# Kernel optimization log

Hardware: AMD Instinct MI355X
Metric: run time of the kernel (lower is better)

Reference implementation:

```python
import jax, jax.numpy as jnp
import numpy as np

EOS_IDX = 2
B, S, T = 512, 64, 32
V, E, H, DENC, L = 128, 256, 512, 1024, 2


def setup_inputs() -> dict:
    key = jax.random.key(0)
    ks = jax.random.split(key, 24)
    s = 0.02
    inp = {
        "encoder_out": jax.random.normal(ks[0], (B, S, DENC), jnp.float32),
        "h0": jax.random.normal(ks[1], (L, B, H), jnp.float32),
        "c0": jax.random.normal(ks[2], (L, B, H), jnp.float32),
        "targets": jax.random.randint(ks[3], (B, T), 0, V),
        "mask": jax.random.randint(ks[4], (B, S), 0, 2).astype(jnp.int32),
        # parameters
        "emb": jax.random.normal(ks[5], (V, E), jnp.float32) * s,
        "W_enc": jax.random.normal(ks[6], (H, DENC), jnp.float32) * s,
        "W_dec": jax.random.normal(ks[7], (H, H), jnp.float32) * s,
        "v": jax.random.normal(ks[8], (H,), jnp.float32) * s,
        "W_ih0": jax.random.normal(ks[9], (4 * H, E + DENC), jnp.float32) * s,
        "W_hh0": jax.random.normal(ks[10], (4 * H, H), jnp.float32) * s,
        "b_ih0": jax.random.normal(ks[11], (4 * H,), jnp.float32) * s,
        "b_hh0": jax.random.normal(ks[12], (4 * H,), jnp.float32) * s,
        "W_ih1": jax.random.normal(ks[13], (4 * H, H), jnp.float32) * s,
        "W_hh1": jax.random.normal(ks[14], (4 * H, H), jnp.float32) * s,
        "b_ih1": jax.random.normal(ks[15], (4 * H,), jnp.float32) * s,
        "b_hh1": jax.random.normal(ks[16], (4 * H,), jnp.float32) * s,
        "W_out": jax.random.normal(ks[17], (V, H + DENC + E), jnp.float32) * s,
        "b_out": jax.random.normal(ks[18], (V,), jnp.float32) * s,
    }
    # guarantee at least one valid source position per row
    inp["mask"] = inp["mask"].at[:, 0].set(1)
    return inp


def _lstm_cell(x, h, c, W_ih, W_hh, b_ih, b_hh):
    gates = x @ W_ih.T + b_ih + h @ W_hh.T + b_hh  # (B, 4H)
    i, f, g, o = jnp.split(gates, 4, axis=-1)      # torch gate order i,f,g,o
    c_new = jax.nn.sigmoid(f) * c + jax.nn.sigmoid(i) * jnp.tanh(g)
    h_new = jax.nn.sigmoid(o) * jnp.tanh(c_new)
    return h_new, c_new


def reference(encoder_out, h0, c0, targets, mask,
              emb, W_enc, W_dec, v,
              W_ih0, W_hh0, b_ih0, b_hh0,
              W_ih1, W_hh1, b_ih1, b_hh1,
              W_out, b_out):
    # teacher_forcing_ratio = 1.0: input tokens are [EOS, targets[:, :-1]]
    tokens = jnp.concatenate(
        [jnp.full((targets.shape[0], 1), EOS_IDX, dtype=targets.dtype),
         targets[:, :-1]], axis=1)                       # (B, T)
    embedded = emb[tokens]                               # (B, T, E)
    enc_proj = jnp.einsum('bsd,hd->bsh', encoder_out, W_enc)  # precompute W_enc(encoder_out)
    mask_b = mask > 0                                    # (B, S)

    def step(carry, x_emb):                              # x_emb: (B, E)
        h, c = carry                                     # each (L, B, H)
        h_top = h[-1]                                    # (B, H)
        dec_proj = h_top @ W_dec.T                       # (B, H)
        energy = jnp.tanh(dec_proj[:, None, :] + enc_proj)   # (B, S, H)
        score = jnp.einsum('bsh,h->bs', energy, v)       # (B, S)
        score = jnp.where(mask_b, score, -jnp.inf)
        weights = jax.nn.softmax(score, axis=-1)         # (B, S)
        context = jnp.einsum('bs,bsd->bd', weights, encoder_out)  # (B, DENC)
        x = jnp.concatenate([x_emb, context], axis=-1)   # (B, E+DENC)
        h0n, c0n = _lstm_cell(x, h[0], c[0], W_ih0, W_hh0, b_ih0, b_hh0)
        h1n, c1n = _lstm_cell(h0n, h[1], c[1], W_ih1, W_hh1, b_ih1, b_hh1)
        pred = jnp.concatenate([h1n, context, x_emb], axis=-1) @ W_out.T + b_out  # (B, V)
        return (jnp.stack([h0n, h1n]), jnp.stack([c0n, c1n])), pred

    (_, _), preds = jax.lax.scan(step, (h0, c0), jnp.swapaxes(embedded, 0, 1))
    return jnp.swapaxes(preds, 0, 1)                     # (B, T, V)
```

## Files before the change

### kernel.cpp

```cpp
#include <hip/hip_runtime.h>
#include <math.h>

#define BB 512
#define SS 64
#define TT 32
#define VV 128
#define EE 256
#define HH 512
#define DENC 1024
#define BH (BB*HH)
#define XW0 1792
#define XW1 1024
#define PW  1792
#define G4H 2048

typedef __attribute__((ext_vector_type(8))) short bf16x8;
typedef __attribute__((ext_vector_type(4))) short bf16x4;
typedef __attribute__((ext_vector_type(4))) float f32x4;

__device__ __forceinline__ float sigf(float x){ return 1.f/(1.f+expf(-x)); }
__device__ __forceinline__ float bf2f(short s){
  return __uint_as_float(((unsigned)(unsigned short)s) << 16);
}
__device__ __forceinline__ short f2bf(float f){
  unsigned u = __float_as_uint(f);
  return (short)((u + 0x7FFF + ((u>>16)&1)) >> 16);
}
__device__ __forceinline__ float tanh_fast(float x){
  x = fminf(fmaxf(x, -15.f), 15.f);
  float e = __expf(2.f*x);
  return (e - 1.f) / (e + 1.f);
}

template<int BM, int BN>
struct GemmPipe {
  static constexpr int LA = 72;
  static __device__ __forceinline__ void run(short* Asb, short* Bsb,
      const short* __restrict__ A, const short* __restrict__ Bt, int K,
      int rowBase, int colBase, int tid, f32x4 acc[BM/32][BN/32])
  {
    constexpr int FI = BM/32, FJ = BN/32, ACH = BM/32, BCH = BN/32;
    const int lane = tid & 63, wave = tid >> 6;
    const int ml = lane & 15, kq = lane >> 4;
    const int wm = (wave >> 1)*(BM/2), wn = (wave & 1)*(BN/2);
    const int arow = (tid*ACH) >> 3, acol = ((tid*ACH) & 7)*8;
    const int brow = (tid*BCH) >> 3, bcol = ((tid*BCH) & 7)*8;
    const short* Ap = A + (size_t)(rowBase+arow)*K + acol;
    const short* Bp = Bt + (size_t)(colBase+brow)*K + bcol;
    bf16x8 ar[ACH], br[BCH];
    #pragma unroll
    for (int c = 0; c < ACH; ++c) ar[c] = *(const bf16x8*)(Ap + c*8);
    #pragma unroll
    for (int c = 0; c < BCH; ++c) br[c] = *(const bf16x8*)(Bp + c*8);
    const int nIter = K >> 6;
    for (int i = 0; i < nIter; ++i) {
      short* Ab = Asb + (i&1)*(BM*LA);
      short* Bb = Bsb + (i&1)*(BN*LA);
      #pragma unroll
      for (int c = 0; c < ACH; ++c) *(bf16x8*)&Ab[arow*LA + acol + c*8] = ar[c];
      #pragma unroll
      for (int c = 0; c < BCH; ++c) *(bf16x8*)&Bb[brow*LA + bcol + c*8] = br[c];
      __syncthreads();
      if (i+1 < nIter) {
        const short* An = Ap + (size_t)(i+1)*64;
        const short* Bn = Bp + (size_t)(i+1)*64;
        #pragma unroll
        for (int c = 0; c < ACH; ++c) ar[c] = *(const bf16x8*)(An + c*8);
        #pragma unroll
        for (int c = 0; c < BCH; ++c) br[c] = *(const bf16x8*)(Bn + c*8);
      }
      #pragma unroll
      for (int kh = 0; kh < 2; ++kh) {
        bf16x8 af[FI], bfv[FJ];
        #pragma unroll
        for (int ii = 0; ii < FI; ++ii)
          af[ii] = *(const bf16x8*)&Ab[(wm + ii*16 + ml)*LA + kh*32 + kq*8];
        #pragma unroll
        for (int jj = 0; jj < FJ; ++jj)
          bfv[jj] = *(const bf16x8*)&Bb[(wn + jj*16 + ml)*LA + kh*32 + kq*8];
        #pragma unroll
        for (int ii = 0; ii < FI; ++ii)
          #pragma unroll
          for (int jj = 0; jj < FJ; ++jj)
            acc[ii][jj] = __builtin_amdgcn_mfma_f32_16x16x32_bf16(af[ii], bfv[jj], acc[ii][jj], 0,0,0);
      }
    }
    __syncthreads();
  }
};

__global__ __launch_bounds__(256)
void gates_fused(const short* __restrict__ A, const short* __restrict__ W,
                 const float* __restrict__ bias, float* __restrict__ cb,
                 short* __restrict__ d1, short* __restrict__ d2, short* __restrict__ d3,
                 int K, int layer)
{
  __shared__ __align__(16) char smem[36864];
  short* As = (short*)smem;
  short* Bs = (short*)(smem + 18432);
  const int tid = threadIdx.x;
  const int rowBase = blockIdx.y*64, colBase = blockIdx.x*64;
  f32x4 acc[2][2];
  #pragma unroll
  for (int i = 0; i < 2; ++i)
    #pragma unroll
    for (int j = 0; j < 2; ++j) acc[i][j] = {0.f,0.f,0.f,0.f};
  GemmPipe<64,64>::run(As, Bs, A, W, K, rowBase, colBase, tid, acc);
  const int lane = tid & 63, wave = tid >> 6, ml = lane & 15, kq = lane >> 4;
  const int wm = (wave >> 1)*32, wn = (wave & 1)*32;
  float* Ct = (float*)smem;
  float bj0 = bias[colBase + wn + ml];
  float bj1 = bias[colBase + wn + 16 + ml];
  #pragma unroll
  for (int ii = 0; ii < 2; ++ii)
    #pragma unroll
    for (int jj = 0; jj < 2; ++jj)
      #pragma unroll
      for (int r2 = 0; r2 < 4; ++r2)
        Ct[(wm + ii*16 + kq*4 + r2)*68 + wn + jj*16 + ml] = acc[ii][jj][r2] + (jj ? bj1 : bj0);
  __syncthreads();
  #pragma unroll
  for (int kk = 0; kk < 4; ++kk) {
    int cidx = tid + kk*256;
    int m = cidx >> 4, hl = cidx & 15;
    float4 gv = *(float4*)&Ct[m*68 + hl*4];
    int b_ = rowBase + m, h_ = (colBase >> 2) + hl;
    float cp = cb[b_*HH + h_];
    float cn = sigf(gv.y)*cp + sigf(gv.x)*tanhf(gv.z);
    float hn = sigf(gv.w)*tanhf(cn);
    cb[b_*HH + h_] = cn;
    short hb16 = f2bf(hn);
    if (layer == 0) {
      d1[(size_t)b_*XW1 + h_] = hb16;
      d2[(size_t)b_*XW0 + h_] = hb16;
    } else {
      d1[(size_t)b_*XW1 + h_] = hb16;
      d2[(size_t)b_*PW  + h_] = hb16;
      d3[(size_t)b_*HH  + h_] = hb16;
    }
  }
}

__global__ __launch_bounds__(256)
void attn_out(const short* __restrict__ enc_proj, const short* __restrict__ enc_out,
              const float* __restrict__ vvec, const int* __restrict__ mask,
              const int* __restrict__ targets, const short* __restrict__ embb,
              const short* __restrict__ hb, const short* __restrict__ wdecT,
              short* __restrict__ xcat0, short* __restrict__ predcat,
              const short* __restrict__ predprev, const short* __restrict__ wout,
              const float* __restrict__ b_out, float* __restrict__ out, int t)
{
  __shared__ __align__(16) char smem[36864];
  const int tid = threadIdx.x;
  if (blockIdx.x >= 256) {
    if (t == 0) return;
    short* As = (short*)smem;
    short* Bs = (short*)(smem + 18432);
    int idx = blockIdx.x - 256;
    int rowBase = (idx >> 1)*64, colBase = (idx & 1)*64;
    f32x4 acc[2][2];
    #pragma unroll
    for (int i = 0; i < 2; ++i)
      #pragma unroll
      for (int j = 0; j < 2; ++j) acc[i][j] = {0.f,0.f,0.f,0.f};
    GemmPipe<64,64>::run(As, Bs, predprev, wout, PW, rowBase, colBase, tid, acc);
    const int lane = tid & 63, wave = tid >> 6, ml = lane & 15, kq = lane >> 4;
    const int wm = (wave >> 1)*32, wn = (wave & 1)*32;
    #pragma unroll
    for (int ii = 0; ii < 2; ++ii)
      #pragma unroll
      for (int jj = 0; jj < 2; ++jj) {
        int n = colBase + wn + jj*16 + ml;
        float bv = b_out[n];
        #pragma unroll
        for (int r2 = 0; r2 < 4; ++r2) {
          int m = rowBase + wm + ii*16 + kq*4 + r2;
          out[(size_t)m*(TT*VV) + (size_t)(t-1)*VV + n] = acc[ii][jj][r2] + bv;
        }
      }
    return;
  }
  if (t >= TT) return;
  const int b0 = blockIdx.x*2;
  float* hbf = (float*)smem;
  float* dps = (float*)(smem + 4096);
  float* vvf = (float*)(smem + 12288);
  float* sc  = (float*)(smem + 14336);
  float* wt  = (float*)(smem + 14848);
  {
    bf16x4 h4 = *(const bf16x4*)&hb[(size_t)b0*HH + tid*4];
    #pragma unroll
    for (int j = 0; j < 4; ++j) hbf[tid*4 + j] = bf2f(h4[j]);
    vvf[tid] = vvec[tid];
    vvf[256 + tid] = vvec[256 + tid];
  }
  __syncthreads();
  {
    int unit = tid & 127, ksel = tid >> 7;
    int bb = unit >> 6, h8 = unit & 63;
    const short* wp = wdecT + (size_t)(ksel*256)*HH + h8*8;
    const float* hrow = hbf + bb*HH + ksel*256;
    float a[8] = {0.f,0.f,0.f,0.f,0.f,0.f,0.f,0.f};
    for (int k = 0; k < 256; ++k) {
      bf16x8 w8 = *(const bf16x8*)(wp + (size_t)k*HH);
      float x = hrow[k];
      #pragma unroll
      for (int j = 0; j < 8; ++j) a[j] += x * bf2f(w8[j]);
    }
    float* d = dps + (ksel*2 + bb)*HH + h8*8;
    #pragma unroll
    for (int j = 0; j < 8; ++j) d[j] = a[j];
  }
  __syncthreads();
  {
    int bb = tid >> 7, h0 = (tid & 127)*4;
    f32x4 s0 = *(f32x4*)&dps[bb*HH + h0];
    f32x4 s1 = *(f32x4*)&dps[(2 + bb)*HH + h0];
    *(f32x4*)&dps[bb*HH + h0] = s0 + s1;
  }
  __syncthreads();
  {
    int u = tid >> 1, khalf = tid & 1;
    int bb = u >> 6, s = u & 63;
    const short* ep = enc_proj + ((size_t)(b0+bb)*SS + s)*HH + khalf*256;
    const float* dpp = dps + bb*HH + khalf*256;
    const float* vp  = vvf + khalf*256;
    float accv = 0.f;
    for (int hc = 0; hc < 32; ++hc) {
      bf16x8 e8 = *(const bf16x8*)(ep + hc*8);
      f32x4 d0 = *(const f32x4*)(dpp + hc*8);
      f32x4 d1 = *(const f32x4*)(dpp + hc*8 + 4);
      f32x4 v0 = *(const f32x4*)(vp + hc*8);
      f32x4 v1 = *(const f32x4*)(vp + hc*8 + 4);
      #pragma unroll
      for (int j = 0; j < 4; ++j) accv += v0[j]*tanh_fast(d0[j] + bf2f(e8[j]));
      #pragma unroll
      for (int j = 0; j < 4; ++j) accv += v1[j]*tanh_fast(d1[j] + bf2f(e8[4+j]));
    }
    accv += __shfl_xor(accv, 1, 64);
    if (khalf == 0) sc[bb*64 + s] = accv;
  }
  __syncthreads();
  if (tid < 128) {
    int bb = tid >> 6, s = tid & 63;
    int valid = mask[(b0+bb)*SS + s];
    float x = valid ? sc[bb*64 + s] : -INFINITY;
    float mx = x;
    #pragma unroll
    for (int off = 32; off; off >>= 1) mx = fmaxf(mx, __shfl_xor(mx, off, 64));
    float e = valid ? __expf(x - mx) : 0.f;
    float sum = e;
    #pragma unroll
    for (int off = 32; off; off >>= 1) sum += __shfl_xor(sum, off, 64);
    wt[bb*64 + s] = e / sum;
  }
  __syncthreads();
  {
    int bb = tid >> 7, d0 = (tid & 127)*8;
    const short* eob = enc_out + (size_t)(b0+bb)*SS*DENC + d0;
    float ca[8] = {0.f,0.f,0.f,0.f,0.f,0.f,0.f,0.f};
    for (int s = 0; s < SS; ++s) {
      float w = wt[bb*64 + s];
      bf16x8 e8 = *(const bf16x8*)(eob + (size_t)s*DENC);
      #pragma unroll
      for (int j = 0; j < 8; ++j) ca[j] += w * bf2f(e8[j]);
    }
    bf16x8 cb8;
    #pragma unroll
    for (int j = 0; j < 8; ++j) cb8[j] = f2bf(ca[j]);
    int b_ = b0 + bb;
    *(bf16x8*)&xcat0[(size_t)b_*XW0 + EE + d0] = cb8;
    *(bf16x8*)&predcat[(size_t)b_*PW + HH + d0] = cb8;
  }
  #pragma unroll
  for (int bb = 0; bb < 2; ++bb) {
    int b_ = b0 + bb;
    int tok = (t == 0) ? 2 : targets[b_*TT + t - 1];
    short ev = embb[tok*EE + tid];
    xcat0[(size_t)b_*XW0 + tid] = ev;
    predcat[(size_t)b_*PW + HH + DENC + tid] = ev;
  }
}

__global__ __launch_bounds__(256)
void enc_gemm(short* __restrict__ C, const short* __restrict__ A, const short* __restrict__ Bt,
              int K, int ldc)
{
  __shared__ __align__(16) char smem[55296];
  short* As = (short*)smem;
  short* Bs = (short*)(smem + 18432);
  const int tid = threadIdx.x;
  const int rowBase = blockIdx.y*64, colBase = blockIdx.x*128;
  f32x4 acc[2][4];
  #pragma unroll
  for (int i = 0; i < 2; ++i)
    #pragma unroll
    for (int j = 0; j < 4; ++j) acc[i][j] = {0.f,0.f,0.f,0.f};
  GemmPipe<64,128>::run(As, Bs, A, Bt, K, rowBase, colBase, tid, acc);
  const int lane = tid & 63, wave = tid >> 6, ml = lane & 15, kq = lane >> 4;
  const int wm = (wave >> 1)*32, wn = (wave & 1)*64;
  #pragma unroll
  for (int ii = 0; ii < 2; ++ii)
    #pragma unroll
    for (int jj = 0; jj < 4; ++jj) {
      int n = colBase + wn + jj*16 + ml;
      #pragma unroll
      for (int r2 = 0; r2 < 4; ++r2) {
        int m = rowBase + wm + ii*16 + kq*4 + r2;
        C[(size_t)m*ldc + n] = f2bf(acc[ii][jj][r2]);
      }
    }
}

__global__ __launch_bounds__(256)
void build_wcat_bf(short* __restrict__ wcat0, short* __restrict__ wcat1,
                   const float* __restrict__ wih0, const float* __restrict__ whh0,
                   const float* __restrict__ wih1, const float* __restrict__ whh1)
{
  int idx = blockIdx.x*256 + threadIdx.x;
  const int N0 = G4H*XW0;
  if (idx < N0) {
    int n = idx / XW0, k = idx % XW0;
    int row = (n & 3)*HH + (n >> 2);
    float v = (k < EE+DENC) ? wih0[(size_t)row*(EE+DENC) + k] : whh0[(size_t)row*HH + (k - (EE+DENC))];
    wcat0[idx] = f2bf(v);
  } else {
    int j = idx - N0;
    int n = j / XW1, k = j % XW1;
    int row = (n & 3)*HH + (n >> 2);
    float v = (k < HH) ? wih1[(size_t)row*HH + k] : whh1[(size_t)row*HH + (k - HH)];
    wcat1[j] = f2bf(v);
  }
}

__global__ __launch_bounds__(256)
void cvt_encout(short* __restrict__ dst, const float* __restrict__ src)
{
  size_t i8 = ((size_t)blockIdx.x*256 + threadIdx.x)*8;
  float4 a = *(const float4*)&src[i8];
  float4 b = *(const float4*)&src[i8+4];
  bf16x8 o;
  o[0]=f2bf(a.x); o[1]=f2bf(a.y); o[2]=f2bf(a.z); o[3]=f2bf(a.w);
  o[4]=f2bf(b.x); o[5]=f2bf(b.y); o[6]=f2bf(b.z); o[7]=f2bf(b.w);
  *(bf16x8*)&dst[i8] = o;
}

__global__ __launch_bounds__(256)
void prep_misc(float* __restrict__ cbuf, short* __restrict__ xcat0a, short* __restrict__ xcat1a,
               short* __restrict__ hb, short* __restrict__ wdecT, short* __restrict__ wenc,
               short* __restrict__ wout, short* __restrict__ embb,
               float* __restrict__ bias0i, float* __restrict__ bias1i,
               const float* __restrict__ c0, const float* __restrict__ h0,
               const float* __restrict__ W_dec, const float* __restrict__ W_enc,
               const float* __restrict__ W_out, const float* __restrict__ emb,
               const float* __restrict__ b_ih0, const float* __restrict__ b_hh0,
               const float* __restrict__ b_ih1, const float* __restrict__ b_hh1)
{
  int idx = blockIdx.x*256 + threadIdx.x;
  if (idx < 524288) { cbuf[idx] = c0[idx]; return; }
  idx -= 524288;
  if (idx < 262144) {
    int b = idx >> 9, h = idx & 511;
    xcat0a[(size_t)b*XW0 + EE + DENC + h] = f2bf(h0[idx]);
    return;
  }
  idx -= 262144;
  if (idx < 262144) {
    int b = idx >> 9, h = idx & 511;
    short v = f2bf(h0[BH + idx]);
    xcat1a[(size_t)b*XW1 + HH + h] = v;
    hb[idx] = v;
    return;
  }
  idx -= 262144;
  if (idx < 262144) {
    int k = idx >> 9, n = idx & 511;
    wdecT[idx] = f2bf(W_dec[(size_t)n*HH + k]);
    return;
  }
  idx -= 262144;
  if (idx < 524288) { wenc[idx] = f2bf(W_enc[idx]); return; }
  idx -= 524288;
  if (idx < 229376) { wout[idx] = f2bf(W_out[idx]); return; }
  idx -= 229376;
  if (idx < 32768)  { embb[idx] = f2bf(emb[idx]); return; }
  idx -= 32768;
  if (idx < 2048) {
    int row = (idx & 3)*HH + (idx >> 2);
    bias0i[idx] = b_ih0[row] + b_hh0[row];
    return;
  }
  idx -= 2048;
  {
    int row = (idx & 3)*HH + (idx >> 2);
    bias1i[idx] = b_ih1[row] + b_hh1[row];
  }
}

extern "C" void kernel_launch(void* const* d_in, const int* in_sizes, int n_in,
                              void* d_out, int out_size, void* d_ws, size_t ws_size,
                              hipStream_t stream) {
  const float* enc_out = (const float*)d_in[0];
  const float* h0      = (const float*)d_in[1];
  const float* c0      = (const float*)d_in[2];
  const int*   targets = (const int*)d_in[3];
  const int*   mask    = (const int*)d_in[4];
  const float* emb     = (const float*)d_in[5];
  const float* W_enc   = (const float*)d_in[6];
  const float* W_dec   = (const float*)d_in[7];
  const float* v       = (const float*)d_in[8];
  const float* b_ih0   = (const float*)d_in[11];
  const float* b_hh0   = (const float*)d_in[12];
  const float* b_ih1   = (const float*)d_in[15];
  const float* b_hh1   = (const float*)d_in[16];
  const float* b_out   = (const float*)d_in[18];
  float* out = (float*)d_out;

  char* ws = (char*)d_ws;
  size_t o = 0;
  short* enc_out_bf = (short*)(ws + o); o += (size_t)BB*SS*DENC*2;
  short* enc_proj_bf= (short*)(ws + o); o += (size_t)BB*SS*HH*2;
  short* wcat0i     = (short*)(ws + o); o += (size_t)G4H*XW0*2;
  short* wcat1i     = (short*)(ws + o); o += (size_t)G4H*XW1*2;
  short* wdecT      = (short*)(ws + o); o += (size_t)HH*HH*2;
  short* wenc_bf    = (short*)(ws + o); o += (size_t)HH*DENC*2;
  short* wout_bf    = (short*)(ws + o); o += (size_t)VV*PW*2;
  short* emb_bf     = (short*)(ws + o); o += (size_t)VV*EE*2;
  short* xcat0a     = (short*)(ws + o); o += (size_t)BB*XW0*2;
  short* xcat0b     = (short*)(ws + o); o += (size_t)BB*XW0*2;
  short* xcat1a     = (short*)(ws + o); o += (size_t)BB*XW1*2;
  short* xcat1b     = (short*)(ws + o); o += (size_t)BB*XW1*2;
  short* predcata   = (short*)(ws + o); o += (size_t)BB*PW*2;
  short* predcatb   = (short*)(ws + o); o += (size_t)BB*PW*2;
  short* hb         = (short*)(ws + o); o += (size_t)BH*2;
  float* cbuf       = (float*)(ws + o); o += (size_t)2*BH*4;
  float* bias0i     = (float*)(ws + o); o += (size_t)G4H*4;
  float* bias1i     = (float*)(ws + o); o += (size_t)G4H*4;
  (void)ws_size; (void)in_sizes; (void)n_in; (void)out_size;

  cvt_encout<<<16384, 256, 0, stream>>>(enc_out_bf, enc_out);
  build_wcat_bf<<<22528, 256, 0, stream>>>(wcat0i, wcat1i,
      (const float*)d_in[9], (const float*)d_in[10], (const float*)d_in[13], (const float*)d_in[14]);
  prep_misc<<<8208, 256, 0, stream>>>(cbuf, xcat0a, xcat1a, hb, wdecT, wenc_bf, wout_bf, emb_bf,
      bias0i, bias1i, c0, h0, W_dec, W_enc, (const float*)d_in[17], emb,
      b_ih0, b_hh0, b_ih1, b_hh1);
  enc_gemm<<<dim3(HH/128, (BB*SS)/64), 256, 0, stream>>>(
      enc_proj_bf, enc_out_bf, wenc_bf, DENC, HH);

  short* xc0[2] = {xcat0a, xcat0b};
  short* xc1[2] = {xcat1a, xcat1b};
  short* pc[2]  = {predcata, predcatb};
  for (int t = 0; t < TT; ++t) {
    attn_out<<<272, 256, 0, stream>>>(enc_proj_bf, enc_out_bf, v, mask, targets, emb_bf,
        hb, wdecT, xc0[t&1], pc[t&1], pc[(t+1)&1], wout_bf, b_out, out, t);
    gates_fused<<<dim3(G4H/64, BB/64), 256, 0, stream>>>(
        xc0[t&1], wcat0i, bias0i, cbuf, xc1[t&1], xc0[(t+1)&1] + EE + DENC, (short*)nullptr, XW0, 0);
    gates_fused<<<dim3(G4H/64, BB/64), 256, 0, stream>>>(
        xc1[t&1], wcat1i, bias1i, cbuf + BH, xc1[(t+1)&1] + HH, pc[t&1], hb, XW1, 1);
  }
  attn_out<<<272, 256, 0, stream>>>(enc_proj_bf, enc_out_bf, v, mask, targets, emb_bf,
      hb, wdecT, xc0[0], pc[0], pc[1], wout_bf, b_out, out, TT);
}
```

Measured before the change: 2.876 ms.

## Split attention into per-row blocks and move output GEMM into layer-0 gates kernel

The attention kernel now uses one 128-thread block per batch row (512 blocks) instead of 256-thread blocks covering two rows each, giving more blocks to spread across CUs. The vocabulary-projection GEMM for the previous step moves from the attention launch into the layer-0 gates launch as 16 extra blocks, and a small final kernel handles the last step. This targets the latency of the serial attention stage, at the cost of reading the W_dec weights once per row instead of once per row pair.

```diff
diff --git a/kernel.cpp b/kernel.cpp
--- a/kernel.cpp
+++ b/kernel.cpp
@@ -36,7 +36,8 @@
 struct GemmPipe {
   static constexpr int LA = 72;
   static __device__ __forceinline__ void run(short* Asb, short* Bsb,
-      const short* __restrict__ A, const short* __restrict__ Bt, int K,
+      const short* __restrict__ A, const short* __restrict__ Bt,
+      int lda, int ldb, int kBase, int nIter,
       int rowBase, int colBase, int tid, f32x4 acc[BM/32][BN/32])
   {
     constexpr int FI = BM/32, FJ = BN/32, ACH = BM/32, BCH = BN/32;
@@ -45,14 +46,13 @@
     const int wm = (wave >> 1)*(BM/2), wn = (wave & 1)*(BN/2);
     const int arow = (tid*ACH) >> 3, acol = ((tid*ACH) & 7)*8;
     const int brow = (tid*BCH) >> 3, bcol = ((tid*BCH) & 7)*8;
-    const short* Ap = A + (size_t)(rowBase+arow)*K + acol;
-    const short* Bp = Bt + (size_t)(colBase+brow)*K + bcol;
+    const short* Ap = A + (size_t)(rowBase+arow)*lda + kBase + acol;
+    const short* Bp = Bt + (size_t)(colBase+brow)*ldb + kBase + bcol;
     bf16x8 ar[ACH], br[BCH];
     #pragma unroll
     for (int c = 0; c < ACH; ++c) ar[c] = *(const bf16x8*)(Ap + c*8);
     #pragma unroll
     for (int c = 0; c < BCH; ++c) br[c] = *(const bf16x8*)(Bp + c*8);
-    const int nIter = K >> 6;
     for (int i = 0; i < nIter; ++i) {
       short* Ab = Asb + (i&1)*(BM*LA);
       short* Bb = Bsb + (i&1)*(BN*LA);
@@ -89,23 +89,170 @@
   }
 };
 
+__device__ __forceinline__ void out_role(int idx, int tid, char* smem,
+    const short* __restrict__ predprev, const short* __restrict__ wout,
+    const float* __restrict__ b_out, float* __restrict__ out, int t)
+{
+  short* As = (short*)smem;
+  short* Bs = (short*)(smem + 18432);
+  const int rowBase = (idx >> 1)*64, colBase = (idx & 1)*64;
+  f32x4 acc[2][2];
+  #pragma unroll
+  for (int i = 0; i < 2; ++i)
+    #pragma unroll
+    for (int j = 0; j < 2; ++j) acc[i][j] = {0.f,0.f,0.f,0.f};
+  GemmPipe<64,64>::run(As, Bs, predprev, wout, PW, PW, 0, PW/64, rowBase, colBase, tid, acc);
+  const int lane = tid & 63, wave = tid >> 6, ml = lane & 15, kq = lane >> 4;
+  const int wm = (wave >> 1)*32, wn = (wave & 1)*32;
+  #pragma unroll
+  for (int ii = 0; ii < 2; ++ii)
+    #pragma unroll
+    for (int jj = 0; jj < 2; ++jj) {
+      int n = colBase + wn + jj*16 + ml;
+      float bv = b_out[n];
+      #pragma unroll
+      for (int r2 = 0; r2 < 4; ++r2) {
+        int m = rowBase + wm + ii*16 + kq*4 + r2;
+        out[(size_t)m*(TT*VV) + (size_t)(t-1)*VV + n] = acc[ii][jj][r2] + bv;
+      }
+    }
+}
+
+__global__ __launch_bounds__(128)
+void attn_row(const short* __restrict__ enc_proj, const short* __restrict__ enc_out,
+              const float* __restrict__ vvec, const int* __restrict__ mask,
+              const int* __restrict__ targets, const short* __restrict__ embb,
+              const short* __restrict__ hb, const short* __restrict__ wdecT,
+              short* __restrict__ xcat0, short* __restrict__ predcat, int t)
+{
+  __shared__ float hbf[512];
+  __shared__ float dps[2][512];
+  __shared__ float vvf[512];
+  __shared__ float sc[64];
+  __shared__ float wt[64];
+  const int tid = threadIdx.x;
+  const int b = blockIdx.x;
+  {
+    bf16x4 h4 = *(const bf16x4*)&hb[(size_t)b*HH + tid*4];
+    #pragma unroll
+    for (int j = 0; j < 4; ++j) hbf[tid*4 + j] = bf2f(h4[j]);
+    vvf[tid]       = vvec[tid];
+    vvf[128 + tid] = vvec[128 + tid];
+    vvf[256 + tid] = vvec[256 + tid];
+    vvf[384 + tid] = vvec[384 + tid];
+  }
+  __syncthreads();
+  {
+    int ksel = tid >> 6, h8 = tid & 63;
+    const short* wp = wdecT + (size_t)(ksel*256)*HH + h8*8;
+    const float* hrow = hbf + ksel*256;
+    float a[8] = {0.f,0.f,0.f,0.f,0.f,0.f,0.f,0.f};
+    #pragma unroll 4
+    for (int k = 0; k < 256; ++k) {
+      bf16x8 w8 = *(const bf16x8*)(wp + (size_t)k*HH);
+      float x = hrow[k];
+      #pragma unroll
+      for (int j = 0; j < 8; ++j) a[j] += x * bf2f(w8[j]);
+    }
+    float* d = dps[ksel] + h8*8;
+    #pragma unroll
+    for (int j = 0; j < 8; ++j) d[j] = a[j];
+  }
+  __syncthreads();
+  {
+    int h0_ = tid*4;
+    f32x4 s0 = *(f32x4*)&dps[0][h0_];
+    f32x4 s1 = *(f32x4*)&dps[1][h0_];
+    *(f32x4*)&dps[0][h0_] = s0 + s1;
+  }
+  __syncthreads();
+  {
+    int s = (tid >> 1) & 63, khalf = tid & 1;
+    const short* ep = enc_proj + ((size_t)b*SS + s)*HH + khalf*256;
+    const float* dpp = dps[0] + khalf*256;
+    const float* vp  = vvf + khalf*256;
+    float accv = 0.f;
+    #pragma unroll 4
+    for (int hc = 0; hc < 32; ++hc) {
+      bf16x8 e8 = *(const bf16x8*)(ep + hc*8);
+      f32x4 d0 = *(const f32x4*)(dpp + hc*8);
+      f32x4 d1 = *(const f32x4*)(dpp + hc*8 + 4);
+      f32x4 v0 = *(const f32x4*)(vp + hc*8);
+      f32x4 v1 = *(const f32x4*)(vp + hc*8 + 4);
+      #pragma unroll
+      for (int j = 0; j < 4; ++j) accv += v0[j]*tanh_fast(d0[j] + bf2f(e8[j]));
+      #pragma unroll
+      for (int j = 0; j < 4; ++j) accv += v1[j]*tanh_fast(d1[j] + bf2f(e8[4+j]));
+    }
+    accv += __shfl_xor(accv, 1, 64);
+    if (khalf == 0) sc[s] = accv;
+  }
+  __syncthreads();
+  if (tid < 64) {
+    int s = tid;
+    int valid = mask[b*SS + s];
+    float x = valid ? sc[s] : -INFINITY;
+    float mx = x;
+    #pragma unroll
+    for (int off = 32; off; off >>= 1) mx = fmaxf(mx, __shfl_xor(mx, off, 64));
+    float e = valid ? __expf(x - mx) : 0.f;
+    float sum = e;
+    #pragma unroll
+    for (int off = 32; off; off >>= 1) sum += __shfl_xor(sum, off, 64);
+    wt[s] = e / sum;
+  }
+  __syncthreads();
+  {
+    int d0 = tid*8;
+    const short* eob = enc_out + (size_t)b*SS*DENC + d0;
+    float ca[8] = {0.f,0.f,0.f,0.f,0.f,0.f,0.f,0.f};
+    #pragma unroll 4
+    for (int s = 0; s < SS; ++s) {
+      float w = wt[s];
+      bf16x8 e8 = *(const bf16x8*)(eob + (size_t)s*DENC);
+      #pragma unroll
+      for (int j = 0; j < 8; ++j) ca[j] += w * bf2f(e8[j]);
+    }
+    bf16x8 cb8;
+    #pragma unroll
+    for (int j = 0; j < 8; ++j) cb8[j] = f2bf(ca[j]);
+    *(bf16x8*)&xcat0[(size_t)b*XW0 + EE + d0] = cb8;
+    *(bf16x8*)&predcat[(size_t)b*PW + HH + d0] = cb8;
+  }
+  {
+    int tok = (t == 0) ? 2 : targets[b*TT + t - 1];
+    short ev0 = embb[tok*EE + tid];
+    short ev1 = embb[tok*EE + 128 + tid];
+    xcat0[(size_t)b*XW0 + tid] = ev0;
+    xcat0[(size_t)b*XW0 + 128 + tid] = ev1;
+    predcat[(size_t)b*PW + HH + DENC + tid] = ev0;
+    predcat[(size_t)b*PW + HH + DENC + 128 + tid] = ev1;
+  }
+}
+
 __global__ __launch_bounds__(256)
 void gates_fused(const short* __restrict__ A, const short* __restrict__ W,
                  const float* __restrict__ bias, float* __restrict__ cb,
                  short* __restrict__ d1, short* __restrict__ d2, short* __restrict__ d3,
-                 int K, int layer)
+                 int K, int layer,
+                 const short* __restrict__ predprev, const short* __restrict__ wout,
+                 const float* __restrict__ b_out, float* __restrict__ out, int t)
 {
   __shared__ __align__(16) char smem[36864];
+  const int tid = threadIdx.x;
+  if (blockIdx.x >= 256) {
+    if (t >= 1) out_role(blockIdx.x - 256, tid, smem, predprev, wout, b_out, out, t);
+    return;
+  }
   short* As = (short*)smem;
   short* Bs = (short*)(smem + 18432);
-  const int tid = threadIdx.x;
-  const int rowBase = blockIdx.y*64, colBase = blockIdx.x*64;
+  const int rowBase = (blockIdx.x >> 5)*64, colBase = (blockIdx.x & 31)*64;
   f32x4 acc[2][2];
   #pragma unroll
   for (int i = 0; i < 2; ++i)
     #pragma unroll
     for (int j = 0; j < 2; ++j) acc[i][j] = {0.f,0.f,0.f,0.f};
-  GemmPipe<64,64>::run(As, Bs, A, W, K, rowBase, colBase, tid, acc);
+  GemmPipe<64,64>::run(As, Bs, A, W, K, K, 0, K >> 6, rowBase, colBase, tid, acc);
   const int lane = tid & 63, wave = tid >> 6, ml = lane & 15, kq = lane >> 4;
   const int wm = (wave >> 1)*32, wn = (wave & 1)*32;
   float* Ct = (float*)smem;
@@ -142,144 +289,11 @@
 }
 
 __global__ __launch_bounds__(256)
-void attn_out(const short* __restrict__ enc_proj, const short* __restrict__ enc_out,
-              const float* __restrict__ vvec, const int* __restrict__ mask,
-              const int* __restrict__ targets, const short* __restrict__ embb,
-              const short* __restrict__ hb, const short* __restrict__ wdecT,
-              short* __restrict__ xcat0, short* __restrict__ predcat,
-              const short* __restrict__ predprev, const short* __restrict__ wout,
-              const float* __restrict__ b_out, float* __restrict__ out, int t)
+void out_fin(const short* __restrict__ predprev, const short* __restrict__ wout,
+             const float* __restrict__ b_out, float* __restrict__ out)
 {
   __shared__ __align__(16) char smem[36864];
-  const int tid = threadIdx.x;
-  if (blockIdx.x >= 256) {
-    if (t == 0) return;
-    short* As = (short*)smem;
-    short* Bs = (short*)(smem + 18432);
-    int idx = blockIdx.x - 256;
-    int rowBase = (idx >> 1)*64, colBase = (idx & 1)*64;
-    f32x4 acc[2][2];
-    #pragma unroll
-    for (int i = 0; i < 2; ++i)
-      #pragma unroll
-      for (int j = 0; j < 2; ++j) acc[i][j] = {0.f,0.f,0.f,0.f};
-    GemmPipe<64,64>::run(As, Bs, predprev, wout, PW, rowBase, colBase, tid, acc);
-    const int lane = tid & 63, wave = tid >> 6, ml = lane & 15, kq = lane >> 4;
-    const int wm = (wave >> 1)*32, wn = (wave & 1)*32;
-    #pragma unroll
-    for (int ii = 0; ii < 2; ++ii)
-      #pragma unroll
-      for (int jj = 0; jj < 2; ++jj) {
-        int n = colBase + wn + jj*16 + ml;
-        float bv = b_out[n];
-        #pragma unroll
-        for (int r2 = 0; r2 < 4; ++r2) {
-          int m = rowBase + wm + ii*16 + kq*4 + r2;
-          out[(size_t)m*(TT*VV) + (size_t)(t-1)*VV + n] = acc[ii][jj][r2] + bv;
-        }
-      }
-    return;
-  }
-  if (t >= TT) return;
-  const int b0 = blockIdx.x*2;
-  float* hbf = (float*)smem;
-  float* dps = (float*)(smem + 4096);
-  float* vvf = (float*)(smem + 12288);
-  float* sc  = (float*)(smem + 14336);
-  float* wt  = (float*)(smem + 14848);
-  {
-    bf16x4 h4 = *(const bf16x4*)&hb[(size_t)b0*HH + tid*4];
-    #pragma unroll
-    for (int j = 0; j < 4; ++j) hbf[tid*4 + j] = bf2f(h4[j]);
-    vvf[tid] = vvec[tid];
-    vvf[256 + tid] = vvec[256 + tid];
-  }
-  __syncthreads();
-  {
-    int unit = tid & 127, ksel = tid >> 7;
-    int bb = unit >> 6, h8 = unit & 63;
-    const short* wp = wdecT + (size_t)(ksel*256)*HH + h8*8;
-    const float* hrow = hbf + bb*HH + ksel*256;
-    float a[8] = {0.f,0.f,0.f,0.f,0.f,0.f,0.f,0.f};
-    for (int k = 0; k < 256; ++k) {
-      bf16x8 w8 = *(const bf16x8*)(wp + (size_t)k*HH);
-      float x = hrow[k];
-      #pragma unroll
-      for (int j = 0; j < 8; ++j) a[j] += x * bf2f(w8[j]);
-    }
-    float* d = dps + (ksel*2 + bb)*HH + h8*8;
-    #pragma unroll
-    for (int j = 0; j < 8; ++j) d[j] = a[j];
-  }
-  __syncthreads();
-  {
-    int bb = tid >> 7, h0 = (tid & 127)*4;
-    f32x4 s0 = *(f32x4*)&dps[bb*HH + h0];
-    f32x4 s1 = *(f32x4*)&dps[(2 + bb)*HH + h0];
-    *(f32x4*)&dps[bb*HH + h0] = s0 + s1;
-  }
-  __syncthreads();
-  {
-    int u = tid >> 1, khalf = tid & 1;
-    int bb = u >> 6, s = u & 63;
-    const short* ep = enc_proj + ((size_t)(b0+bb)*SS + s)*HH + khalf*256;
-    const float* dpp = dps + bb*HH + khalf*256;
-    const float* vp  = vvf + khalf*256;
-    float accv = 0.f;
-    for (int hc = 0; hc < 32; ++hc) {
-      bf16x8 e8 = *(const bf16x8*)(ep + hc*8);
-      f32x4 d0 = *(const f32x4*)(dpp + hc*8);
-      f32x4 d1 = *(const f32x4*)(dpp + hc*8 + 4);
-      f32x4 v0 = *(const f32x4*)(vp + hc*8);
-      f32x4 v1 = *(const f32x4*)(vp + hc*8 + 4);
-      #pragma unroll
-      for (int j = 0; j < 4; ++j) accv += v0[j]*tanh_fast(d0[j] + bf2f(e8[j]));
-      #pragma unroll
-      for (int j = 0; j < 4; ++j) accv += v1[j]*tanh_fast(d1[j] + bf2f(e8[4+j]));
-    }
-    accv += __shfl_xor(accv, 1, 64);
-    if (khalf == 0) sc[bb*64 + s] = accv;
-  }
-  __syncthreads();
-  if (tid < 128) {
-    int bb = tid >> 6, s = tid & 63;
-    int valid = mask[(b0+bb)*SS + s];
-    float x = valid ? sc[bb*64 + s] : -INFINITY;
-    float mx = x;
-    #pragma unroll
-    for (int off = 32; off; off >>= 1) mx = fmaxf(mx, __shfl_xor(mx, off, 64));
-    float e = valid ? __expf(x - mx) : 0.f;
-    float sum = e;
-    #pragma unroll
-    for (int off = 32; off; off >>= 1) sum += __shfl_xor(sum, off, 64);
-    wt[bb*64 + s] = e / sum;
-  }
-  __syncthreads();
-  {
-    int bb = tid >> 7, d0 = (tid & 127)*8;
-    const short* eob = enc_out + (size_t)(b0+bb)*SS*DENC + d0;
-    float ca[8] = {0.f,0.f,0.f,0.f,0.f,0.f,0.f,0.f};
-    for (int s = 0; s < SS; ++s) {
-      float w = wt[bb*64 + s];
-      bf16x8 e8 = *(const bf16x8*)(eob + (size_t)s*DENC);
-      #pragma unroll
-      for (int j = 0; j < 8; ++j) ca[j] += w * bf2f(e8[j]);
-    }
-    bf16x8 cb8;
-    #pragma unroll
-    for (int j = 0; j < 8; ++j) cb8[j] = f2bf(ca[j]);
-    int b_ = b0 + bb;
-    *(bf16x8*)&xcat0[(size_t)b_*XW0 + EE + d0] = cb8;
-    *(bf16x8*)&predcat[(size_t)b_*PW + HH + d0] = cb8;
-  }
-  #pragma unroll
-  for (int bb = 0; bb < 2; ++bb) {
-    int b_ = b0 + bb;
-    int tok = (t == 0) ? 2 : targets[b_*TT + t - 1];
-    short ev = embb[tok*EE + tid];
-    xcat0[(size_t)b_*XW0 + tid] = ev;
-    predcat[(size_t)b_*PW + HH + DENC + tid] = ev;
-  }
+  out_role(blockIdx.x, threadIdx.x, smem, predprev, wout, b_out, out, TT);
 }
 
 __global__ __launch_bounds__(256)
@@ -296,7 +310,7 @@
   for (int i = 0; i < 2; ++i)
     #pragma unroll
     for (int j = 0; j < 4; ++j) acc[i][j] = {0.f,0.f,0.f,0.f};
-  GemmPipe<64,128>::run(As, Bs, A, Bt, K, rowBase, colBase, tid, acc);
+  GemmPipe<64,128>::run(As, Bs, A, Bt, K, K, 0, K >> 6, rowBase, colBase, tid, acc);
   const int lane = tid & 63, wave = tid >> 6, ml = lane & 15, kq = lane >> 4;
   const int wm = (wave >> 1)*32, wn = (wave & 1)*64;
   #pragma unroll
@@ -451,13 +465,15 @@
   short* xc1[2] = {xcat1a, xcat1b};
   short* pc[2]  = {predcata, predcatb};
   for (int t = 0; t < TT; ++t) {
-    attn_out<<<272, 256, 0, stream>>>(enc_proj_bf, enc_out_bf, v, mask, targets, emb_bf,
-        hb, wdecT, xc0[t&1], pc[t&1], pc[(t+1)&1], wout_bf, b_out, out, t);
-    gates_fused<<<dim3(G4H/64, BB/64), 256, 0, stream>>>(
-        xc0[t&1], wcat0i, bias0i, cbuf, xc1[t&1], xc0[(t+1)&1] + EE + DENC, (short*)nullptr, XW0, 0);
-    gates_fused<<<dim3(G4H/64, BB/64), 256, 0, stream>>>(
-        xc1[t&1], wcat1i, bias1i, cbuf + BH, xc1[(t+1)&1] + HH, pc[t&1], hb, XW1, 1);
-  }
-  attn_out<<<272, 256, 0, stream>>>(enc_proj_bf, enc_out_bf, v, mask, targets, emb_bf,
-      hb, wdecT, xc0[0], pc[0], pc[1], wout_bf, b_out, out, TT);
-}
+    attn_row<<<512, 128, 0, stream>>>(enc_proj_bf, enc_out_bf, v, mask, targets, emb_bf,
+        hb, wdecT, xc0[t&1], pc[t&1], t);
+    gates_fused<<<272, 256, 0, stream>>>(
+        xc0[t&1], wcat0i, bias0i, cbuf, xc1[t&1], xc0[(t+1)&1] + EE + DENC, (short*)nullptr,
+        XW0, 0, pc[(t+1)&1], wout_bf, b_out, out, t);
+    gates_fused<<<256, 256, 0, stream>>>(
+        xc1[t&1], wcat1i, bias1i, cbuf + BH, xc1[(t+1)&1] + HH, pc[t&1], hb,
+        XW1, 1, (const short*)nullptr, (const short*)nullptr, (const float*)nullptr,
+        (float*)nullptr, 0);
+  }
+  out_fin<<<16, 256, 0, stream>>>(pc[1], wout_bf, b_out, out);
+}
```

After: 3.108 ms. 8.1% more time.

## Overlap attention-independent layer-0 gate GEMM slices with attention kernel

Applied to the files above, without the earlier changes.

The layer-0 gate GEMM is split along K. The embedding and previous-hidden slices are computed by extra blocks inside the attention launch and stored as fp32 partials. A follow-up kernel adds only the context slice and applies the LSTM epilogue. Next-step embeddings are prewritten by extra blocks, and the initial EOS embedding moves into setup. The aim is to fill idle CUs during attention and shorten the critical path, at the cost of an extra partial-sum round trip through global memory.

```diff
diff --git a/kernel.cpp b/kernel.cpp
--- a/kernel.cpp
+++ b/kernel.cpp
@@ -32,11 +32,19 @@
   return (e - 1.f) / (e + 1.f);
 }
 
+__device__ __forceinline__ void zacc(f32x4 a[2][2]){
+  #pragma unroll
+  for (int i = 0; i < 2; ++i)
+    #pragma unroll
+    for (int j = 0; j < 2; ++j) a[i][j] = {0.f,0.f,0.f,0.f};
+}
+
 template<int BM, int BN>
 struct GemmPipe {
   static constexpr int LA = 72;
   static __device__ __forceinline__ void run(short* Asb, short* Bsb,
-      const short* __restrict__ A, const short* __restrict__ Bt, int K,
+      const short* __restrict__ A, const short* __restrict__ Bt,
+      int lda, int ldb, int kBase, int nIter,
       int rowBase, int colBase, int tid, f32x4 acc[BM/32][BN/32])
   {
     constexpr int FI = BM/32, FJ = BN/32, ACH = BM/32, BCH = BN/32;
@@ -45,14 +53,13 @@
     const int wm = (wave >> 1)*(BM/2), wn = (wave & 1)*(BN/2);
     const int arow = (tid*ACH) >> 3, acol = ((tid*ACH) & 7)*8;
     const int brow = (tid*BCH) >> 3, bcol = ((tid*BCH) & 7)*8;
-    const short* Ap = A + (size_t)(rowBase+arow)*K + acol;
-    const short* Bp = Bt + (size_t)(colBase+brow)*K + bcol;
+    const short* Ap = A + (size_t)(rowBase+arow)*lda + kBase + acol;
+    const short* Bp = Bt + (size_t)(colBase+brow)*ldb + kBase + bcol;
     bf16x8 ar[ACH], br[BCH];
     #pragma unroll
     for (int c = 0; c < ACH; ++c) ar[c] = *(const bf16x8*)(Ap + c*8);
     #pragma unroll
     for (int c = 0; c < BCH; ++c) br[c] = *(const bf16x8*)(Bp + c*8);
-    const int nIter = K >> 6;
     for (int i = 0; i < nIter; ++i) {
       short* Ab = Asb + (i&1)*(BM*LA);
       short* Bb = Bsb + (i&1)*(BN*LA);
@@ -89,99 +96,15 @@
   }
 };
 
-__global__ __launch_bounds__(256)
-void gates_fused(const short* __restrict__ A, const short* __restrict__ W,
-                 const float* __restrict__ bias, float* __restrict__ cb,
-                 short* __restrict__ d1, short* __restrict__ d2, short* __restrict__ d3,
-                 int K, int layer)
-{
-  __shared__ __align__(16) char smem[36864];
-  short* As = (short*)smem;
-  short* Bs = (short*)(smem + 18432);
-  const int tid = threadIdx.x;
-  const int rowBase = blockIdx.y*64, colBase = blockIdx.x*64;
-  f32x4 acc[2][2];
-  #pragma unroll
-  for (int i = 0; i < 2; ++i)
-    #pragma unroll
-    for (int j = 0; j < 2; ++j) acc[i][j] = {0.f,0.f,0.f,0.f};
-  GemmPipe<64,64>::run(As, Bs, A, W, K, rowBase, colBase, tid, acc);
-  const int lane = tid & 63, wave = tid >> 6, ml = lane & 15, kq = lane >> 4;
-  const int wm = (wave >> 1)*32, wn = (wave & 1)*32;
-  float* Ct = (float*)smem;
-  float bj0 = bias[colBase + wn + ml];
-  float bj1 = bias[colBase + wn + 16 + ml];
-  #pragma unroll
-  for (int ii = 0; ii < 2; ++ii)
-    #pragma unroll
-    for (int jj = 0; jj < 2; ++jj)
-      #pragma unroll
-      for (int r2 = 0; r2 < 4; ++r2)
-        Ct[(wm + ii*16 + kq*4 + r2)*68 + wn + jj*16 + ml] = acc[ii][jj][r2] + (jj ? bj1 : bj0);
-  __syncthreads();
-  #pragma unroll
-  for (int kk = 0; kk < 4; ++kk) {
-    int cidx = tid + kk*256;
-    int m = cidx >> 4, hl = cidx & 15;
-    float4 gv = *(float4*)&Ct[m*68 + hl*4];
-    int b_ = rowBase + m, h_ = (colBase >> 2) + hl;
-    float cp = cb[b_*HH + h_];
-    float cn = sigf(gv.y)*cp + sigf(gv.x)*tanhf(gv.z);
-    float hn = sigf(gv.w)*tanhf(cn);
-    cb[b_*HH + h_] = cn;
-    short hb16 = f2bf(hn);
-    if (layer == 0) {
-      d1[(size_t)b_*XW1 + h_] = hb16;
-      d2[(size_t)b_*XW0 + h_] = hb16;
-    } else {
-      d1[(size_t)b_*XW1 + h_] = hb16;
-      d2[(size_t)b_*PW  + h_] = hb16;
-      d3[(size_t)b_*HH  + h_] = hb16;
-    }
-  }
-}
-
-__global__ __launch_bounds__(256)
-void attn_out(const short* __restrict__ enc_proj, const short* __restrict__ enc_out,
-              const float* __restrict__ vvec, const int* __restrict__ mask,
-              const int* __restrict__ targets, const short* __restrict__ embb,
-              const short* __restrict__ hb, const short* __restrict__ wdecT,
-              short* __restrict__ xcat0, short* __restrict__ predcat,
-              const short* __restrict__ predprev, const short* __restrict__ wout,
-              const float* __restrict__ b_out, float* __restrict__ out, int t)
-{
-  __shared__ __align__(16) char smem[36864];
-  const int tid = threadIdx.x;
-  if (blockIdx.x >= 256) {
-    if (t == 0) return;
-    short* As = (short*)smem;
-    short* Bs = (short*)(smem + 18432);
-    int idx = blockIdx.x - 256;
-    int rowBase = (idx >> 1)*64, colBase = (idx & 1)*64;
-    f32x4 acc[2][2];
-    #pragma unroll
-    for (int i = 0; i < 2; ++i)
-      #pragma unroll
-      for (int j = 0; j < 2; ++j) acc[i][j] = {0.f,0.f,0.f,0.f};
-    GemmPipe<64,64>::run(As, Bs, predprev, wout, PW, rowBase, colBase, tid, acc);
-    const int lane = tid & 63, wave = tid >> 6, ml = lane & 15, kq = lane >> 4;
-    const int wm = (wave >> 1)*32, wn = (wave & 1)*32;
-    #pragma unroll
-    for (int ii = 0; ii < 2; ++ii)
-      #pragma unroll
-      for (int jj = 0; jj < 2; ++jj) {
-        int n = colBase + wn + jj*16 + ml;
-        float bv = b_out[n];
-        #pragma unroll
-        for (int r2 = 0; r2 < 4; ++r2) {
-          int m = rowBase + wm + ii*16 + kq*4 + r2;
-          out[(size_t)m*(TT*VV) + (size_t)(t-1)*VV + n] = acc[ii][jj][r2] + bv;
-        }
-      }
-    return;
-  }
-  if (t >= TT) return;
-  const int b0 = blockIdx.x*2;
+
+__device__ __forceinline__ void attn_role(int aid, int tid, char* smem, int t,
+    const short* __restrict__ enc_proj, const short* __restrict__ enc_out,
+    const float* __restrict__ vvec, const int* __restrict__ mask,
+    const int* __restrict__ targets, const short* __restrict__ embb,
+    const short* __restrict__ hb, const short* __restrict__ wdecT,
+    short* __restrict__ xcat0, short* __restrict__ predcat)
+{
+  const int b0 = aid*2;
   float* hbf = (float*)smem;
   float* dps = (float*)(smem + 4096);
   float* vvf = (float*)(smem + 12288);
@@ -213,10 +136,10 @@
   }
   __syncthreads();
   {
-    int bb = tid >> 7, h0 = (tid & 127)*4;
-    f32x4 s0 = *(f32x4*)&dps[bb*HH + h0];
-    f32x4 s1 = *(f32x4*)&dps[(2 + bb)*HH + h0];
-    *(f32x4*)&dps[bb*HH + h0] = s0 + s1;
+    int bb = tid >> 7, h0_ = (tid & 127)*4;
+    f32x4 s0 = *(f32x4*)&dps[bb*HH + h0_];
+    f32x4 s1 = *(f32x4*)&dps[(2 + bb)*HH + h0_];
+    *(f32x4*)&dps[bb*HH + h0_] = s0 + s1;
   }
   __syncthreads();
   {
@@ -276,10 +199,184 @@
   for (int bb = 0; bb < 2; ++bb) {
     int b_ = b0 + bb;
     int tok = (t == 0) ? 2 : targets[b_*TT + t - 1];
-    short ev = embb[tok*EE + tid];
-    xcat0[(size_t)b_*XW0 + tid] = ev;
-    predcat[(size_t)b_*PW + HH + DENC + tid] = ev;
-  }
+    predcat[(size_t)b_*PW + HH + DENC + tid] = embb[tok*EE + tid];
+  }
+}
+
+__device__ __forceinline__ void out_role(int idx, int tid, char* smem,
+    const short* __restrict__ predprev, const short* __restrict__ wout,
+    const float* __restrict__ b_out, float* __restrict__ out, int t)
+{
+  short* As = (short*)smem;
+  short* Bs = (short*)(smem + 18432);
+  const int rowBase = (idx >> 1)*64, colBase = (idx & 1)*64;
+  f32x4 acc[2][2];
+  zacc(acc);
+  GemmPipe<64,64>::run(As, Bs, predprev, wout, PW, PW, 0, PW/64, rowBase, colBase, tid, acc);
+  const int lane = tid & 63, wave = tid >> 6, ml = lane & 15, kq = lane >> 4;
+  const int wm = (wave >> 1)*32, wn = (wave & 1)*32;
+  #pragma unroll
+  for (int ii = 0; ii < 2; ++ii)
+    #pragma unroll
+    for (int jj = 0; jj < 2; ++jj) {
+      int n = colBase + wn + jj*16 + ml;
+      float bv = b_out[n];
+      #pragma unroll
+      for (int r2 = 0; r2 < 4; ++r2) {
+        int m = rowBase + wm + ii*16 + kq*4 + r2;
+        out[(size_t)m*(TT*VV) + (size_t)(t-1)*VV + n] = acc[ii][jj][r2] + bv;
+      }
+    }
+}
+
+__device__ __forceinline__ void pstore(int tid, int rowBase, int colBase,
+    float* __restrict__ P, f32x4 acc[2][2])
+{
+  const int lane = tid & 63, wave = tid >> 6, ml = lane & 15, kq = lane >> 4;
+  const int wm = (wave >> 1)*32, wn = (wave & 1)*32;
+  #pragma unroll
+  for (int ii = 0; ii < 2; ++ii)
+    #pragma unroll
+    for (int jj = 0; jj < 2; ++jj)
+      #pragma unroll
+      for (int r2 = 0; r2 < 4; ++r2)
+        P[(size_t)(rowBase + wm + ii*16 + kq*4 + r2)*G4H + colBase + wn + jj*16 + ml] = acc[ii][jj][r2];
+}
+
+__device__ __forceinline__ void gates_epi(int tid, int rowBase, int colBase,
+    char* smem, f32x4 acc[2][2], const float* __restrict__ bias,
+    float* __restrict__ cb,
+    short* __restrict__ d1, int ld1, short* __restrict__ d2, int ld2,
+    short* __restrict__ d3)
+{
+  const int lane = tid & 63, wave = tid >> 6, ml = lane & 15, kq = lane >> 4;
+  const int wm = (wave >> 1)*32, wn = (wave & 1)*32;
+  float* Ct = (float*)smem;
+  float bj0 = bias[colBase + wn + ml];
+  float bj1 = bias[colBase + wn + 16 + ml];
+  #pragma unroll
+  for (int ii = 0; ii < 2; ++ii)
+    #pragma unroll
+    for (int jj = 0; jj < 2; ++jj)
+      #pragma unroll
+      for (int r2 = 0; r2 < 4; ++r2)
+        Ct[(wm + ii*16 + kq*4 + r2)*68 + wn + jj*16 + ml] = acc[ii][jj][r2] + (jj ? bj1 : bj0);
+  __syncthreads();
+  #pragma unroll
+  for (int kk = 0; kk < 4; ++kk) {
+    int cidx = tid + kk*256;
+    int m = cidx >> 4, hl = cidx & 15;
+    float4 gv = *(float4*)&Ct[m*68 + hl*4];
+    int b_ = rowBase + m, h_ = (colBase >> 2) + hl;
+    float cp = cb[b_*HH + h_];
+    float cn = sigf(gv.y)*cp + sigf(gv.x)*tanhf(gv.z);
+    float hn = sigf(gv.w)*tanhf(cn);
+    cb[b_*HH + h_] = cn;
+    short hb16 = f2bf(hn);
+    d1[(size_t)b_*ld1 + h_] = hb16;
+    d2[(size_t)b_*ld2 + h_] = hb16;
+    if (d3) d3[(size_t)b_*HH + h_] = hb16;
+  }
+}
+
+__device__ __forceinline__ void emb_prewrite(int rowBase, int tid,
+    short* __restrict__ xc0n, const int* __restrict__ targets,
+    const short* __restrict__ embb, int t)
+{
+  int b_ = rowBase + (tid >> 2);
+  int tok = targets[b_*TT + t];
+  const short* src = embb + tok*EE + (tid & 3)*64;
+  short* dst = xc0n + (size_t)b_*XW0 + (tid & 3)*64;
+  #pragma unroll
+  for (int j = 0; j < 8; ++j)
+    *(bf16x8*)(dst + j*8) = *(const bf16x8*)(src + j*8);
+}
+
+
+__global__ __launch_bounds__(256)
+void attn_pg0(const short* __restrict__ enc_proj, const short* __restrict__ enc_out,
+              const float* __restrict__ vvec, const int* __restrict__ mask,
+              const int* __restrict__ targets, const short* __restrict__ embb,
+              const short* __restrict__ hb, const short* __restrict__ wdecT,
+              short* __restrict__ xcat0, short* __restrict__ predcat,
+              const short* __restrict__ wcat0, float* __restrict__ P0,
+              const short* __restrict__ predprev, const short* __restrict__ wout,
+              const float* __restrict__ b_out, float* __restrict__ out, int t)
+{
+  __shared__ __align__(16) char smem[36864];
+  const int tid = threadIdx.x, bid = blockIdx.x;
+  if (bid < 256) {
+    attn_role(bid, tid, smem, t, enc_proj, enc_out, vvec, mask, targets,
+              embb, hb, wdecT, xcat0, predcat);
+  } else if (bid < 512) {
+    short* As = (short*)smem;
+    short* Bs = (short*)(smem + 18432);
+    int idx = bid - 256;
+    int rowBase = (idx >> 5)*64, colBase = (idx & 31)*64;
+    f32x4 acc[2][2];
+    zacc(acc);
+    GemmPipe<64,64>::run(As, Bs, xcat0, wcat0, XW0, XW0, 0,    4, rowBase, colBase, tid, acc);
+    GemmPipe<64,64>::run(As, Bs, xcat0, wcat0, XW0, XW0, 1280, 8, rowBase, colBase, tid, acc);
+    pstore(tid, rowBase, colBase, P0, acc);
+  } else {
+    if (t >= 1) out_role(bid - 512, tid, smem, predprev, wout, b_out, out, t);
+  }
+}
+
+__global__ __launch_bounds__(256)
+void gates0_fin(const short* __restrict__ A, const short* __restrict__ W,
+                const float* __restrict__ bias, const float* __restrict__ P0,
+                float* __restrict__ cb,
+                short* __restrict__ d1, short* __restrict__ d2,
+                short* __restrict__ xc0n, const int* __restrict__ targets,
+                const short* __restrict__ embb, int t)
+{
+  __shared__ __align__(16) char smem[36864];
+  const int tid = threadIdx.x, bid = blockIdx.x;
+  if (bid >= 256) {
+    if (t + 1 < TT) emb_prewrite((bid - 256)*64, tid, xc0n, targets, embb, t);
+    return;
+  }
+  short* As = (short*)smem;
+  short* Bs = (short*)(smem + 18432);
+  const int rowBase = (bid >> 5)*64, colBase = (bid & 31)*64;
+  const int lane = tid & 63, wave = tid >> 6, ml = lane & 15, kq = lane >> 4;
+  const int wm = (wave >> 1)*32, wn = (wave & 1)*32;
+  f32x4 acc[2][2];
+  const float* Pp = P0 + (size_t)rowBase*G4H + colBase;
+  #pragma unroll
+  for (int ii = 0; ii < 2; ++ii)
+    #pragma unroll
+    for (int jj = 0; jj < 2; ++jj)
+      #pragma unroll
+      for (int r2 = 0; r2 < 4; ++r2)
+        acc[ii][jj][r2] = Pp[(wm + ii*16 + kq*4 + r2)*G4H + wn + jj*16 + ml];
+  GemmPipe<64,64>::run(As, Bs, A, W, XW0, XW0, 256, 16, rowBase, colBase, tid, acc);
+  gates_epi(tid, rowBase, colBase, smem, acc, bias, cb, d1, XW1, d2, XW0, (short*)nullptr);
+}
+
+__global__ __launch_bounds__(256)
+void gates1_full(const short* __restrict__ A, const short* __restrict__ W,
+                 const float* __restrict__ bias, float* __restrict__ cb,
+                 short* __restrict__ d1, short* __restrict__ d2, short* __restrict__ d3)
+{
+  __shared__ __align__(16) char smem[36864];
+  const int tid = threadIdx.x, bid = blockIdx.x;
+  short* As = (short*)smem;
+  short* Bs = (short*)(smem + 18432);
+  const int rowBase = (bid >> 5)*64, colBase = (bid & 31)*64;
+  f32x4 acc[2][2];
+  zacc(acc);
+  GemmPipe<64,64>::run(As, Bs, A, W, XW1, XW1, 0, 16, rowBase, colBase, tid, acc);
+  gates_epi(tid, rowBase, colBase, smem, acc, bias, cb, d1, XW1, d2, PW, d3);
+}
+
+__global__ __launch_bounds__(256)
+void out_fin(const short* __restrict__ predprev, const short* __restrict__ wout,
+             const float* __restrict__ b_out, float* __restrict__ out)
+{
+  __shared__ __align__(16) char smem[36864];
+  out_role(blockIdx.x, threadIdx.x, smem, predprev, wout, b_out, out, TT);
 }
 
 __global__ __launch_bounds__(256)
@@ -296,7 +393,7 @@
   for (int i = 0; i < 2; ++i)
     #pragma unroll
     for (int j = 0; j < 4; ++j) acc[i][j] = {0.f,0.f,0.f,0.f};
-  GemmPipe<64,128>::run(As, Bs, A, Bt, K, rowBase, colBase, tid, acc);
+  GemmPipe<64,128>::run(As, Bs, A, Bt, K, K, 0, K >> 6, rowBase, colBase, tid, acc);
   const int lane = tid & 63, wave = tid >> 6, ml = lane & 15, kq = lane >> 4;
   const int wm = (wave >> 1)*32, wn = (wave & 1)*64;
   #pragma unroll
@@ -391,9 +488,15 @@
     return;
   }
   idx -= 2048;
-  {
+  if (idx < 2048) {
     int row = (idx & 3)*HH + (idx >> 2);
     bias1i[idx] = b_ih1[row] + b_hh1[row];
+    return;
+  }
+  idx -= 2048;
+  {
+    int b = idx >> 8, e = idx & 255;
+    xcat0a[(size_t)b*XW0 + e] = f2bf(emb[2*EE + e]);
   }
 }
 
@@ -436,12 +539,13 @@
   float* cbuf       = (float*)(ws + o); o += (size_t)2*BH*4;
   float* bias0i     = (float*)(ws + o); o += (size_t)G4H*4;
   float* bias1i     = (float*)(ws + o); o += (size_t)G4H*4;
+  float* P0         = (float*)(ws + o); o += (size_t)BB*G4H*4;
   (void)ws_size; (void)in_sizes; (void)n_in; (void)out_size;
 
   cvt_encout<<<16384, 256, 0, stream>>>(enc_out_bf, enc_out);
   build_wcat_bf<<<22528, 256, 0, stream>>>(wcat0i, wcat1i,
       (const float*)d_in[9], (const float*)d_in[10], (const float*)d_in[13], (const float*)d_in[14]);
-  prep_misc<<<8208, 256, 0, stream>>>(cbuf, xcat0a, xcat1a, hb, wdecT, wenc_bf, wout_bf, emb_bf,
+  prep_misc<<<8720, 256, 0, stream>>>(cbuf, xcat0a, xcat1a, hb, wdecT, wenc_bf, wout_bf, emb_bf,
       bias0i, bias1i, c0, h0, W_dec, W_enc, (const float*)d_in[17], emb,
       b_ih0, b_hh0, b_ih1, b_hh1);
   enc_gemm<<<dim3(HH/128, (BB*SS)/64), 256, 0, stream>>>(
@@ -451,13 +555,13 @@
   short* xc1[2] = {xcat1a, xcat1b};
   short* pc[2]  = {predcata, predcatb};
   for (int t = 0; t < TT; ++t) {
-    attn_out<<<272, 256, 0, stream>>>(enc_proj_bf, enc_out_bf, v, mask, targets, emb_bf,
-        hb, wdecT, xc0[t&1], pc[t&1], pc[(t+1)&1], wout_bf, b_out, out, t);
-    gates_fused<<<dim3(G4H/64, BB/64), 256, 0, stream>>>(
-        xc0[t&1], wcat0i, bias0i, cbuf, xc1[t&1], xc0[(t+1)&1] + EE + DENC, (short*)nullptr, XW0, 0);
-    gates_fused<<<dim3(G4H/64, BB/64), 256, 0, stream>>>(
-        xc1[t&1], wcat1i, bias1i, cbuf + BH, xc1[(t+1)&1] + HH, pc[t&1], hb, XW1, 1);
-  }
-  attn_out<<<272, 256, 0, stream>>>(enc_proj_bf, enc_out_bf, v, mask, targets, emb_bf,
-      hb, wdecT, xc0[0], pc[0], pc[1], wout_bf, b_out, out, TT);
-}
+    attn_pg0<<<528, 256, 0, stream>>>(enc_proj_bf, enc_out_bf, v, mask, targets, emb_bf,
+        hb, wdecT, xc0[t&1], pc[t&1], wcat0i, P0, pc[(t+1)&1], wout_bf, b_out, out, t);
+    gates0_fin<<<264, 256, 0, stream>>>(
+        xc0[t&1], wcat0i, bias0i, P0, cbuf, xc1[t&1], xc0[(t+1)&1] + EE + DENC,
+        xc0[(t+1)&1], targets, emb_bf, t);
+    gates1_full<<<256, 256, 0, stream>>>(
+        xc1[t&1], wcat1i, bias1i, cbuf + BH, xc1[(t+1)&1] + HH, pc[t&1], hb);
+  }
+  out_fin<<<16, 256, 0, stream>>>(pc[1], wout_bf, b_out, out);
+}
```

Measured after the change: 2.797 ms. 2.8% less time.
